# Kernel tuning notes

Measured on AMD Instinct MI355X. Metric: run time of the kernel, lower is better.

Reference implementation:

```python
import jax, jax.numpy as jnp
import numpy as np
import math

N_HEADS = 16
EMBD = 1024
D_HEAD = EMBD // N_HEADS


def setup_inputs() -> dict:
    key = jax.random.key(0)
    ks = jax.random.split(key, 5)
    s = 1.0 / math.sqrt(EMBD)
    return {
        "x": jax.random.normal(ks[0], (2, 2048, EMBD), dtype=jnp.float32),
        "w_in": jax.random.normal(ks[1], (EMBD, 3 * EMBD), dtype=jnp.float32) * s,
        "b_in": jax.random.normal(ks[2], (3 * EMBD,), dtype=jnp.float32) * 0.02,
        "w_out": jax.random.normal(ks[3], (EMBD, EMBD), dtype=jnp.float32) * s,
        "b_out": jax.random.normal(ks[4], (EMBD,), dtype=jnp.float32) * 0.02,
    }


def reference(x, w_in, b_in, w_out, b_out):
    # x: [B, S, D]
    B, S, D = x.shape
    qkv = x @ w_in + b_in                      # [B, S, 3D]
    q, k, v = jnp.split(qkv, 3, axis=-1)
    # [B, S, H, dh] -> [B, H, S, dh]
    def heads(t):
        return t.reshape(B, S, N_HEADS, D_HEAD).transpose(0, 2, 1, 3)
    q, k, v = heads(q), heads(k), heads(v)
    scores = jnp.einsum("bhqd,bhkd->bhqk", q, k)  # [B, H, S, S]
    # causal mask applied before scaling (as in original; -inf invariant to scale)
    causal = jnp.tril(jnp.ones((S, S), dtype=bool))
    scores = jnp.where(causal, scores, -jnp.inf)
    scores = scores / jnp.asarray(math.sqrt(D_HEAD), dtype=scores.dtype)
    attn = jax.nn.softmax(scores, axis=-1)
    out = jnp.einsum("bhqk,bhkd->bhqd", attn, v)  # [B, H, S, dh]
    out = out.transpose(0, 2, 1, 3).reshape(B, S, D)
    return out @ w_out + b_out
```

## Files before the change

### kernel.cpp

```cpp
#include <hip/hip_runtime.h>
#include <stdint.h>

#define DEVI __device__ __forceinline__

typedef __attribute__((ext_vector_type(8))) short short8;
typedef __attribute__((ext_vector_type(4))) float f32x4;
typedef __attribute__((ext_vector_type(4))) uint32_t u32x4;

DEVI unsigned short f2bf(float f) {
    union { float f; uint32_t u; } v; v.f = f;
    return (unsigned short)((v.u + 0x7FFFu + ((v.u >> 16) & 1u)) >> 16);
}

DEVI uint32_t cvtpk_bf16(float a, float b) {
    uint32_t r;
    asm("v_cvt_pk_bf16_f32 %0, %1, %2" : "=v"(r) : "v"(a), "v"(b));
    return r;
}

DEVI void perm32(uint32_t &a, uint32_t &b) {
    asm("v_permlane32_swap_b32 %0, %1" : "+v"(a), "+v"(b));
}
DEVI void perm16(uint32_t &a, uint32_t &b) {
    asm("v_permlane16_swap_b32 %0, %1" : "+v"(a), "+v"(b));
}

DEVI void gload16(const void* g, void* l) {
    __builtin_amdgcn_global_load_lds(
        (const __attribute__((address_space(1))) unsigned int*)g,
        (__attribute__((address_space(3))) unsigned int*)l, 16, 0, 0);
}

__global__ void k_cvt(const float* __restrict__ in, ushort* __restrict__ out, int n4) {
    int i = blockIdx.x * blockDim.x + threadIdx.x;
    int stride = gridDim.x * blockDim.x;
    for (; i < n4; i += stride) {
        float4 v = ((const float4*)in)[i];
        ushort4 o;
        o.x = f2bf(v.x); o.y = f2bf(v.y); o.z = f2bf(v.z); o.w = f2bf(v.w);
        ((ushort4*)out)[i] = o;
    }
}

__global__ void k_tcvt(const float* __restrict__ in, ushort* __restrict__ out, int R, int C) {
    __shared__ float t[32][33];
    int c0 = blockIdx.x * 32, r0 = blockIdx.y * 32;
    int lr = threadIdx.x >> 5, lc = threadIdx.x & 31;
    #pragma unroll
    for (int i = 0; i < 4; i++)
        t[lr + 8*i][lc] = in[(size_t)(r0 + lr + 8*i)*C + c0 + lc];
    __syncthreads();
    #pragma unroll
    for (int i = 0; i < 4; i++)
        out[(size_t)(c0 + lr + 8*i)*R + r0 + lc] = f2bf(t[lc][lr + 8*i]);
}

template<int MODE>
__global__ __launch_bounds__(256, 2) void k_gemm(
    const ushort* __restrict__ A, const ushort* __restrict__ Bt,
    const float* __restrict__ bias,
    ushort* __restrict__ oQ, ushort* __restrict__ oK, ushort* __restrict__ oV,
    float* __restrict__ oF,
    int M, int N, int K, int S)
{
    __shared__ __align__(16) ushort As[128*64];
    __shared__ __align__(16) ushort Bs[128*64];
    const int tid = threadIdx.x;
    const int w = tid >> 6, l = tid & 63;

    int lin = blockIdx.y * gridDim.x + blockIdx.x;
    int nwg = gridDim.x * gridDim.y;
    int swz = (lin & 7) * (nwg >> 3) + (lin >> 3);
    const int m0 = (swz / gridDim.x) * 128, n0 = (swz % gridDim.x) * 128;

    const int wr = (w >> 1) * 64, wc = (w & 1) * 64;
    const int fr = l & 15, fg = l >> 4;
    const int lr8 = l >> 3;
    const int slot = (l & 7) ^ lr8;

    f32x4 acc[4][4] = {};

    const ushort* Abase = A + (size_t)(m0 + w*32 + lr8) * K + slot*8;
    const ushort* Bbase = Bt + (size_t)(n0 + w*32 + lr8) * K + slot*8;

    for (int k0 = 0; k0 < K; k0 += 64) {
        __syncthreads();
        #pragma unroll
        for (int i = 0; i < 4; i++) {
            gload16(Abase + (size_t)(8*i)*K + k0, &As[(w*32 + 8*i)*64]);
            gload16(Bbase + (size_t)(8*i)*K + k0, &Bs[(w*32 + 8*i)*64]);
        }
        __syncthreads();
        #pragma unroll
        for (int kk = 0; kk < 2; kk++) {
            short8 af[4], bfr[4];
            #pragma unroll
            for (int i = 0; i < 4; i++) {
                int ra = wr + i*16 + fr;
                af[i] = *(const short8*)((const char*)As + ra*128 + ((kk*64 + fg*16) ^ ((ra & 7) << 4)));
                int rb = wc + i*16 + fr;
                bfr[i] = *(const short8*)((const char*)Bs + rb*128 + ((kk*64 + fg*16) ^ ((rb & 7) << 4)));
            }
            #pragma unroll
            for (int i = 0; i < 4; i++)
                #pragma unroll
                for (int j = 0; j < 4; j++)
                    acc[i][j] = __builtin_amdgcn_mfma_f32_16x16x32_bf16(af[i], bfr[j], acc[i][j], 0, 0, 0);
        }
    }

    if (MODE == 1) {
        #pragma unroll
        for (int j = 0; j < 4; j++) {
            int n = n0 + wc + j*16 + fr;
            float bv = bias[n];
            #pragma unroll
            for (int i = 0; i < 4; i++) {
                int mrow = m0 + wr + i*16 + fg*4;
                #pragma unroll
                for (int r = 0; r < 4; r++)
                    oF[(size_t)(mrow + r)*N + n] = acc[i][j][r] + bv;
            }
        }
    } else {
        #pragma unroll
        for (int j = 0; j < 4; j++) {
            int n = n0 + wc + j*16 + fr;
            int region = n >> 10;
            int h = (n & 1023) >> 6;
            int d = n & 63;
            float bv = bias[n];
            float scl = (region == 0) ? 0.18033688011112042f : 1.0f;
            #pragma unroll
            for (int i = 0; i < 4; i++) {
                int mrow = m0 + wr + i*16 + fg*4;
                int b = mrow >> 11;
                int s = mrow & 2047;
                if (region < 2) {
                    ushort* dst = (region == 0 ? oQ : oK) + ((size_t)(b*16 + h)*S)*64 + (size_t)d;
                    #pragma unroll
                    for (int r = 0; r < 4; r++)
                        dst[(size_t)(s + r)*64] = f2bf((acc[i][j][r] + bv) * scl);
                } else {
                    ushort* dst = oV + ((size_t)(b*16 + h)*64 + d)*S + s;
                    ushort4 pk;
                    pk.x = f2bf(acc[i][j][0] + bv);
                    pk.y = f2bf(acc[i][j][1] + bv);
                    pk.z = f2bf(acc[i][j][2] + bv);
                    pk.w = f2bf(acc[i][j][3] + bv);
                    *(ushort4*)dst = pk;
                }
            }
        }
    }
}

__global__ __launch_bounds__(128, 2) void k_attn(
    const ushort* __restrict__ Q,
    const ushort* __restrict__ Kb,
    const ushort* __restrict__ Vt,
    ushort* __restrict__ O,
    int S)
{
    __shared__ __align__(16) ushort Kt[2][64*64];
    __shared__ __align__(16) ushort Vs[2][64*64];

    const int tid = threadIdx.x, w = tid >> 6, l = tid & 63;
    const int bid = blockIdx.x;
    const int half = bid >> 9;
    const int r_ = bid & 511;
    const int h = r_ & 15, b = (r_ >> 4) & 1, p = r_ >> 5;
    const int qt = half ? p : (31 - p);
    const int bh = b * 16 + h;
    const int qw = qt * 64 + w * 32;
    const int fr = l & 15, fg = l >> 4;

    short8 qf[2][2];
    {
        const ushort* qp = Q + ((size_t)bh*S + qw + fr)*64 + fg*8;
        qf[0][0] = *(const short8*)(qp);
        qf[0][1] = *(const short8*)(qp + 32);
        qf[1][0] = *(const short8*)(qp + 16*64);
        qf[1][1] = *(const short8*)(qp + 16*64 + 32);
    }

    float l_[2] = {0.f, 0.f};
    f32x4 o_[2][4] = {};

    const int lr8 = l >> 3;
    const int slot = (l & 7) ^ lr8;
    const ushort* Ksrc = Kb + (size_t)bh*S*64;
    const ushort* Vsrc = Vt + (size_t)bh*64*S;

    const int nt = qt + 1;

    auto stage = [&](int buf, int j0) {
        #pragma unroll
        for (int i = 0; i < 4; i++) {
            int rb = w*32 + i*8;
            gload16(Ksrc + (size_t)(j0 + rb + lr8)*64 + slot*8, &Kt[buf][rb*64]);
            gload16(Vsrc + (size_t)(rb + lr8)*S + j0 + slot*8, &Vs[buf][rb*64]);
        }
    };

    stage(0, 0);
    __syncthreads();
    int cur = 0;

    for (int jt = 0; jt < nt; jt++) {
        const int j0 = jt * 64;
        if (jt + 1 < nt) stage(cur ^ 1, j0 + 64);

        f32x4 sa[2][4] = {};
        __builtin_amdgcn_s_setprio(1);
        #pragma unroll
        for (int kk = 0; kk < 2; kk++) {
            short8 kf[4];
            #pragma unroll
            for (int f = 0; f < 4; f++) {
                int row = f*16 + fr;
                kf[f] = *(const short8*)((const char*)Kt[cur] + row*128 + ((kk*64 + fg*16) ^ ((row & 7) << 4)));
            }
            #pragma unroll
            for (int t = 0; t < 2; t++)
                #pragma unroll
                for (int f = 0; f < 4; f++)
                    sa[t][f] = __builtin_amdgcn_mfma_f32_16x16x32_bf16(kf[f], qf[t][kk], sa[t][f], 0, 0, 0);
        }
        __builtin_amdgcn_s_setprio(0);

        if (jt == nt - 1) {
            #pragma unroll
            for (int t = 0; t < 2; t++) {
                int qg = qw + t*16 + fr;
                #pragma unroll
                for (int f = 0; f < 4; f++) {
                    int base = j0 + f*16 + fg*4 - qg;
                    #pragma unroll
                    for (int r = 0; r < 4; r++)
                        if (base + r > 0) sa[t][f][r] = -1e30f;
                }
            }
        }

        uint32_t cw[2][4][2];
        #pragma unroll
        for (int t = 0; t < 2; t++)
            #pragma unroll
            for (int f = 0; f < 4; f++) {
                float p0 = __builtin_amdgcn_exp2f(sa[t][f][0]);
                float p1 = __builtin_amdgcn_exp2f(sa[t][f][1]);
                float p2 = __builtin_amdgcn_exp2f(sa[t][f][2]);
                float p3 = __builtin_amdgcn_exp2f(sa[t][f][3]);
                l_[t] += (p0 + p1) + (p2 + p3);
                cw[t][f][0] = cvtpk_bf16(p0, p1);
                cw[t][f][1] = cvtpk_bf16(p2, p3);
            }

        __builtin_amdgcn_s_setprio(1);
        #pragma unroll
        for (int kk = 0; kk < 2; kk++) {
            short8 pf[2];
            #pragma unroll
            for (int t = 0; t < 2; t++) {
                uint32_t a0 = cw[t][2*kk][0], b0 = cw[t][2*kk + 1][0];
                perm32(a0, b0); perm16(a0, b0);
                uint32_t a1 = cw[t][2*kk][1], b1 = cw[t][2*kk + 1][1];
                perm32(a1, b1); perm16(a1, b1);
                u32x4 uw; uw[0] = a0; uw[1] = a1; uw[2] = b0; uw[3] = b1;
                pf[t] = __builtin_bit_cast(short8, uw);
            }
            #pragma unroll
            for (int f = 0; f < 4; f++) {
                int row = f*16 + fr;
                short8 vf = *(const short8*)((const char*)Vs[cur] + row*128 + ((kk*64 + fg*16) ^ ((row & 7) << 4)));
                #pragma unroll
                for (int t = 0; t < 2; t++)
                    o_[t][f] = __builtin_amdgcn_mfma_f32_16x16x32_bf16(vf, pf[t], o_[t][f], 0, 0, 0);
            }
        }
        __builtin_amdgcn_s_setprio(0);

        __syncthreads();
        cur ^= 1;
    }

    #pragma unroll
    for (int t = 0; t < 2; t++) {
        l_[t] += __shfl_xor(l_[t], 16);
        l_[t] += __shfl_xor(l_[t], 32);
    }

    #pragma unroll
    for (int t = 0; t < 2; t++) {
        float inv = 1.0f / l_[t];
        int qg = qw + t*16 + fr;
        #pragma unroll
        for (int f = 0; f < 4; f++) {
            ushort4 pk;
            pk.x = f2bf(o_[t][f][0] * inv);
            pk.y = f2bf(o_[t][f][1] * inv);
            pk.z = f2bf(o_[t][f][2] * inv);
            pk.w = f2bf(o_[t][f][3] * inv);
            *(ushort4*)&O[((size_t)(b*S + qg))*1024 + h*64 + f*16 + fg*4] = pk;
        }
    }
}

extern "C" void kernel_launch(void* const* d_in, const int* in_sizes, int n_in,
                              void* d_out, int out_size, void* d_ws, size_t ws_size,
                              hipStream_t stream)
{
    const float* x     = (const float*)d_in[0];
    const float* w_in  = (const float*)d_in[1];
    const float* b_in  = (const float*)d_in[2];
    const float* w_out = (const float*)d_in[3];
    const float* b_out = (const float*)d_in[4];
    float* out = (float*)d_out;

    const int B = 2, S = 2048, D = 1024, H = 16;
    const int M = B * S;

    if (ws_size < (40u << 20)) return;
    char* ws = (char*)d_ws;
    ushort* xb     = (ushort*)(ws);
    ushort* w_inT  = (ushort*)(ws + (8u << 20));
    ushort* w_outT = (ushort*)(ws + (14u << 20));
    ushort* qb     = (ushort*)(ws + (16u << 20));
    ushort* kb     = (ushort*)(ws + (24u << 20));
    ushort* vtb    = (ushort*)(ws + (32u << 20));

    k_cvt<<<2048, 256, 0, stream>>>(x, xb, M*D/4);
    k_tcvt<<<dim3(3*D/32, D/32), 256, 0, stream>>>(w_in, w_inT, D, 3*D);
    k_tcvt<<<dim3(D/32, D/32), 256, 0, stream>>>(w_out, w_outT, D, D);
    k_gemm<0><<<dim3(3*D/128, M/128), 256, 0, stream>>>(xb, w_inT, b_in, qb, kb, vtb, nullptr, M, 3*D, D, S);
    k_attn<<<1024, 128, 0, stream>>>(qb, kb, vtb, xb, S);
    k_gemm<1><<<dim3(D/128, M/128), 256, 0, stream>>>(xb, w_outT, b_out, nullptr, nullptr, nullptr, out, M, D, D, S);
}
```

Measured before the change: 110.9 us.

## Split attention KV range across two blocks and combine partials in a separate kernel

```diff
diff --git a/kernel.cpp b/kernel.cpp
--- a/kernel.cpp
+++ b/kernel.cpp
@@ -159,21 +159,23 @@
     const ushort* __restrict__ Q,
     const ushort* __restrict__ Kb,
     const ushort* __restrict__ Vt,
-    ushort* __restrict__ O,
+    float* __restrict__ po,
+    float* __restrict__ pl,
     int S)
 {
     __shared__ __align__(16) ushort Kt[2][64*64];
-    __shared__ __align__(16) ushort Vs[2][64*64];
 
     const int tid = threadIdx.x, w = tid >> 6, l = tid & 63;
     const int bid = blockIdx.x;
-    const int half = bid >> 9;
-    const int r_ = bid & 511;
-    const int h = r_ & 15, b = (r_ >> 4) & 1, p = r_ >> 5;
-    const int qt = half ? p : (31 - p);
-    const int bh = b * 16 + h;
+    const int bh = bid & 31;
+    const int c = (bid >> 5) & 1;
+    const int qt = 31 - (bid >> 6);
     const int qw = qt * 64 + w * 32;
     const int fr = l & 15, fg = l >> 4;
+
+    const int len0 = (qt + 2) >> 1;
+    const int t0 = c ? len0 : 0;
+    const int t1 = c ? (qt + 1) : len0;
 
     short8 qf[2][2];
     {
@@ -192,24 +194,28 @@
     const ushort* Ksrc = Kb + (size_t)bh*S*64;
     const ushort* Vsrc = Vt + (size_t)bh*64*S;
 
-    const int nt = qt + 1;
-
     auto stage = [&](int buf, int j0) {
         #pragma unroll
         for (int i = 0; i < 4; i++) {
             int rb = w*32 + i*8;
             gload16(Ksrc + (size_t)(j0 + rb + lr8)*64 + slot*8, &Kt[buf][rb*64]);
-            gload16(Vsrc + (size_t)(rb + lr8)*S + j0 + slot*8, &Vs[buf][rb*64]);
         }
     };
 
-    stage(0, 0);
+    if (t0 < t1) stage(0, t0 * 64);
     __syncthreads();
     int cur = 0;
 
-    for (int jt = 0; jt < nt; jt++) {
+    for (int jt = t0; jt < t1; jt++) {
         const int j0 = jt * 64;
-        if (jt + 1 < nt) stage(cur ^ 1, j0 + 64);
+        if (jt + 1 < t1) stage(cur ^ 1, j0 + 64);
+
+        short8 vf[2][4];
+        #pragma unroll
+        for (int kk = 0; kk < 2; kk++)
+            #pragma unroll
+            for (int f = 0; f < 4; f++)
+                vf[kk][f] = *(const short8*)(Vsrc + (size_t)(f*16 + fr)*S + j0 + kk*32 + fg*8);
 
         f32x4 sa[2][4] = {};
         __builtin_amdgcn_s_setprio(1);
@@ -229,7 +235,7 @@
         }
         __builtin_amdgcn_s_setprio(0);
 
-        if (jt == nt - 1) {
+        if (jt == qt) {
             #pragma unroll
             for (int t = 0; t < 2; t++) {
                 int qg = qw + t*16 + fr;
@@ -271,13 +277,10 @@
                 pf[t] = __builtin_bit_cast(short8, uw);
             }
             #pragma unroll
-            for (int f = 0; f < 4; f++) {
-                int row = f*16 + fr;
-                short8 vf = *(const short8*)((const char*)Vs[cur] + row*128 + ((kk*64 + fg*16) ^ ((row & 7) << 4)));
+            for (int f = 0; f < 4; f++)
                 #pragma unroll
                 for (int t = 0; t < 2; t++)
-                    o_[t][f] = __builtin_amdgcn_mfma_f32_16x16x32_bf16(vf, pf[t], o_[t][f], 0, 0, 0);
-            }
+                    o_[t][f] = __builtin_amdgcn_mfma_f32_16x16x32_bf16(vf[kk][f], pf[t], o_[t][f], 0, 0, 0);
         }
         __builtin_amdgcn_s_setprio(0);
 
@@ -291,19 +294,45 @@
         l_[t] += __shfl_xor(l_[t], 32);
     }
 
+    float* pob = po + ((size_t)bid * 2 + w) * 2048;
     #pragma unroll
     for (int t = 0; t < 2; t++) {
-        float inv = 1.0f / l_[t];
-        int qg = qw + t*16 + fr;
-        #pragma unroll
-        for (int f = 0; f < 4; f++) {
-            ushort4 pk;
-            pk.x = f2bf(o_[t][f][0] * inv);
-            pk.y = f2bf(o_[t][f][1] * inv);
-            pk.z = f2bf(o_[t][f][2] * inv);
-            pk.w = f2bf(o_[t][f][3] * inv);
-            *(ushort4*)&O[((size_t)(b*S + qg))*1024 + h*64 + f*16 + fg*4] = pk;
-        }
+        #pragma unroll
+        for (int f = 0; f < 4; f++)
+            *(f32x4*)&pob[(((t*4 + f)*16 + fr)*4 + fg)*4] = o_[t][f];
+        if (fg == 0) pl[(size_t)bid*64 + w*32 + t*16 + fr] = l_[t];
+    }
+}
+
+__global__ __launch_bounds__(256) void k_comb(
+    const float* __restrict__ po, const float* __restrict__ pl,
+    ushort* __restrict__ O, int S)
+{
+    const int bx = blockIdx.x;
+    const int qt = bx >> 5, bh = bx & 31;
+    const int b = bh >> 4, h = bh & 15;
+    const int iA = ((31 - qt) << 6) | bh;
+    const int iB = iA | 32;
+    const f32x4* pa = (const f32x4*)(po + (size_t)iA * 4096);
+    const f32x4* pb = (const f32x4*)(po + (size_t)iB * 4096);
+    const float* la = pl + (size_t)iA * 64;
+    const float* lb = pl + (size_t)iB * 64;
+
+    #pragma unroll
+    for (int k = 0; k < 4; k++) {
+        int ss = threadIdx.x + 256 * k;
+        int w = (ss >> 9) & 1, t = (ss >> 8) & 1, f = (ss >> 6) & 3, fr = (ss >> 2) & 15, fg = ss & 3;
+        int row = w*32 + t*16 + fr;
+        f32x4 a = pa[ss], c = pb[ss];
+        float den = fmaxf(la[row] + lb[row], 1e-30f);
+        float inv = 1.0f / den;
+        ushort4 pk;
+        pk.x = f2bf((a[0] + c[0]) * inv);
+        pk.y = f2bf((a[1] + c[1]) * inv);
+        pk.z = f2bf((a[2] + c[2]) * inv);
+        pk.w = f2bf((a[3] + c[3]) * inv);
+        int q = qt*64 + row;
+        *(ushort4*)&O[((size_t)(b*S + q))*1024 + h*64 + f*16 + fg*4] = pk;
     }
 }
 
@@ -321,7 +350,7 @@
     const int B = 2, S = 2048, D = 1024, H = 16;
     const int M = B * S;
 
-    if (ws_size < (40u << 20)) return;
+    if (ws_size < (80u << 20)) return;
     char* ws = (char*)d_ws;
     ushort* xb     = (ushort*)(ws);
     ushort* w_inT  = (ushort*)(ws + (8u << 20));
@@ -329,11 +358,14 @@
     ushort* qb     = (ushort*)(ws + (16u << 20));
     ushort* kb     = (ushort*)(ws + (24u << 20));
     ushort* vtb    = (ushort*)(ws + (32u << 20));
+    float*  po     = (float*)(ws + (40u << 20));
+    float*  pl     = (float*)(ws + (75u << 20));
 
     k_cvt<<<2048, 256, 0, stream>>>(x, xb, M*D/4);
     k_tcvt<<<dim3(3*D/32, D/32), 256, 0, stream>>>(w_in, w_inT, D, 3*D);
     k_tcvt<<<dim3(D/32, D/32), 256, 0, stream>>>(w_out, w_outT, D, D);
     k_gemm<0><<<dim3(3*D/128, M/128), 256, 0, stream>>>(xb, w_inT, b_in, qb, kb, vtb, nullptr, M, 3*D, D, S);
-    k_attn<<<1024, 128, 0, stream>>>(qb, kb, vtb, xb, S);
+    k_attn<<<2048, 128, 0, stream>>>(qb, kb, vtb, po, pl, S);
+    k_comb<<<1024, 256, 0, stream>>>(po, pl, xb, S);
     k_gemm<1><<<dim3(D/128, M/128), 256, 0, stream>>>(xb, w_outT, b_out, nullptr, nullptr, nullptr, out, M, D, D, S);
 }
```

Measured after the change: 120.4 us. 8.6% more time.

## Pipeline GEMM loads with triple/double-buffered LDS and larger QKV tiles

Applied to the files above, without the earlier changes.

```diff
diff --git a/kernel.cpp b/kernel.cpp
--- a/kernel.cpp
+++ b/kernel.cpp
@@ -55,60 +55,104 @@
         out[(size_t)(c0 + lr + 8*i)*R + r0 + lc] = f2bf(t[lc][lr + 8*i]);
 }
 
-template<int MODE>
-__global__ __launch_bounds__(256, 2) void k_gemm(
+template<int MODE, int MW, int NW>
+__global__ __launch_bounds__(MW*NW*64, 2) void k_gemm2(
     const ushort* __restrict__ A, const ushort* __restrict__ Bt,
     const float* __restrict__ bias,
     ushort* __restrict__ oQ, ushort* __restrict__ oK, ushort* __restrict__ oV,
     float* __restrict__ oF,
     int M, int N, int K, int S)
 {
-    __shared__ __align__(16) ushort As[128*64];
-    __shared__ __align__(16) ushort Bs[128*64];
+    constexpr int THREADS = MW*NW*64;
+    constexpr int BM = MW*64, BN = NW*64;
+    constexpr int ACALLS = 8/NW;
+    constexpr int BCALLS = 8/MW;
+    constexpr int RPC = THREADS/8;
+    __shared__ __align__(16) ushort As[3*BM*64];
+    __shared__ __align__(16) ushort Bs[2*BN*64];
+
     const int tid = threadIdx.x;
     const int w = tid >> 6, l = tid & 63;
+    const int wm = w / NW, wn = w % NW;
 
     int lin = blockIdx.y * gridDim.x + blockIdx.x;
     int nwg = gridDim.x * gridDim.y;
     int swz = (lin & 7) * (nwg >> 3) + (lin >> 3);
-    const int m0 = (swz / gridDim.x) * 128, n0 = (swz % gridDim.x) * 128;
-
-    const int wr = (w >> 1) * 64, wc = (w & 1) * 64;
+    const int m0 = (swz / gridDim.x) * BM, n0 = (swz % gridDim.x) * BN;
+
     const int fr = l & 15, fg = l >> 4;
     const int lr8 = l >> 3;
     const int slot = (l & 7) ^ lr8;
 
+    const int NT = K >> 6;
+
     f32x4 acc[4][4] = {};
 
-    const ushort* Abase = A + (size_t)(m0 + w*32 + lr8) * K + slot*8;
-    const ushort* Bbase = Bt + (size_t)(n0 + w*32 + lr8) * K + slot*8;
-
-    for (int k0 = 0; k0 < K; k0 += 64) {
-        __syncthreads();
+    const ushort* Ab = A + (size_t)(m0 + w*8 + lr8) * K + slot*8;
+    const ushort* Bb = Bt + (size_t)(n0 + w*8 + lr8) * K + slot*8;
+
+    auto stageA = [&](int sl, int kt) {
+        const ushort* src = Ab + (size_t)kt * 64;
+        #pragma unroll
+        for (int c = 0; c < ACALLS; c++)
+            gload16(src + (size_t)(c*RPC)*K, &As[sl*(BM*64) + (c*RPC + w*8)*64]);
+    };
+    auto stageB = [&](int sl, int kt) {
+        const ushort* src = Bb + (size_t)kt * 64;
+        #pragma unroll
+        for (int c = 0; c < BCALLS; c++)
+            gload16(src + (size_t)(c*RPC)*K, &Bs[sl*(BN*64) + (c*RPC + w*8)*64]);
+    };
+
+    stageA(0, 0);
+    stageB(0, 0);
+    if (NT > 1) stageA(1, 1); else stageA(1, 0);
+
+    for (int t = 0; t < NT; t++) {
+        asm volatile("s_waitcnt vmcnt(4)" ::: "memory");
+        __builtin_amdgcn_s_barrier();
+        __builtin_amdgcn_sched_barrier(0);
+
+        const char* Asl = (const char*)As + (size_t)(t % 3) * (BM*64) * 2;
+        const char* Bsl = (const char*)Bs + (size_t)(t & 1) * (BN*64) * 2;
+
+        short8 af[4], bf[4];
         #pragma unroll
         for (int i = 0; i < 4; i++) {
-            gload16(Abase + (size_t)(8*i)*K + k0, &As[(w*32 + 8*i)*64]);
-            gload16(Bbase + (size_t)(8*i)*K + k0, &Bs[(w*32 + 8*i)*64]);
-        }
-        __syncthreads();
-        #pragma unroll
-        for (int kk = 0; kk < 2; kk++) {
-            short8 af[4], bfr[4];
-            #pragma unroll
-            for (int i = 0; i < 4; i++) {
-                int ra = wr + i*16 + fr;
-                af[i] = *(const short8*)((const char*)As + ra*128 + ((kk*64 + fg*16) ^ ((ra & 7) << 4)));
-                int rb = wc + i*16 + fr;
-                bfr[i] = *(const short8*)((const char*)Bs + rb*128 + ((kk*64 + fg*16) ^ ((rb & 7) << 4)));
-            }
-            #pragma unroll
-            for (int i = 0; i < 4; i++)
-                #pragma unroll
-                for (int j = 0; j < 4; j++)
-                    acc[i][j] = __builtin_amdgcn_mfma_f32_16x16x32_bf16(af[i], bfr[j], acc[i][j], 0, 0, 0);
-        }
-    }
-
+            int ra = wm*64 + i*16 + fr;
+            af[i] = *(const short8*)(Asl + ra*128 + ((fg*16) ^ ((ra & 7) << 4)));
+            int rb = wn*64 + i*16 + fr;
+            bf[i] = *(const short8*)(Bsl + rb*128 + ((fg*16) ^ ((rb & 7) << 4)));
+        }
+        stageB((t + 1) & 1, (t + 1 < NT) ? t + 1 : 0);
+        __builtin_amdgcn_s_setprio(1);
+        #pragma unroll
+        for (int i = 0; i < 4; i++)
+            #pragma unroll
+            for (int j = 0; j < 4; j++)
+                acc[i][j] = __builtin_amdgcn_mfma_f32_16x16x32_bf16(af[i], bf[j], acc[i][j], 0, 0, 0);
+        __builtin_amdgcn_s_setprio(0);
+
+        #pragma unroll
+        for (int i = 0; i < 4; i++) {
+            int ra = wm*64 + i*16 + fr;
+            af[i] = *(const short8*)(Asl + ra*128 + ((64 + fg*16) ^ ((ra & 7) << 4)));
+            int rb = wn*64 + i*16 + fr;
+            bf[i] = *(const short8*)(Bsl + rb*128 + ((64 + fg*16) ^ ((rb & 7) << 4)));
+        }
+        stageA((t + 2) % 3, (t + 2 < NT) ? t + 2 : 0);
+        __builtin_amdgcn_s_setprio(1);
+        #pragma unroll
+        for (int i = 0; i < 4; i++)
+            #pragma unroll
+            for (int j = 0; j < 4; j++)
+                acc[i][j] = __builtin_amdgcn_mfma_f32_16x16x32_bf16(af[i], bf[j], acc[i][j], 0, 0, 0);
+        __builtin_amdgcn_s_setprio(0);
+    }
+
+    asm volatile("s_waitcnt vmcnt(0)" ::: "memory");
+
+    const int wr = wm*64, wc = wn*64;
     if (MODE == 1) {
         #pragma unroll
         for (int j = 0; j < 4; j++) {
@@ -333,7 +377,7 @@
     k_cvt<<<2048, 256, 0, stream>>>(x, xb, M*D/4);
     k_tcvt<<<dim3(3*D/32, D/32), 256, 0, stream>>>(w_in, w_inT, D, 3*D);
     k_tcvt<<<dim3(D/32, D/32), 256, 0, stream>>>(w_out, w_outT, D, D);
-    k_gemm<0><<<dim3(3*D/128, M/128), 256, 0, stream>>>(xb, w_inT, b_in, qb, kb, vtb, nullptr, M, 3*D, D, S);
+    k_gemm2<0,4,2><<<dim3(3*D/128, M/256), 512, 0, stream>>>(xb, w_inT, b_in, qb, kb, vtb, nullptr, M, 3*D, D, S);
     k_attn<<<1024, 128, 0, stream>>>(qb, kb, vtb, xb, S);
-    k_gemm<1><<<dim3(D/128, M/128), 256, 0, stream>>>(xb, w_outT, b_out, nullptr, nullptr, nullptr, out, M, D, D, S);
-}
+    k_gemm2<1,2,2><<<dim3(D/128, M/128), 256, 0, stream>>>(xb, w_outT, b_out, nullptr, nullptr, nullptr, out, M, D, D, S);
+}
```

Measured after the change: 122.1 us. 10.2% more time.
